# Kernel tuning notes

Hardware: AMD Instinct MI355X
Metric: run time of the kernel (lower is better)

Reference implementation:

```python
import jax, jax.numpy as jnp
import numpy as np

N = 1024          # n noisy tokens (seq = 2*N)
DIM = 768
HEADS = 12
HD = DIM // HEADS
BLOCK = 16        # diffusion block size
COND = 128
DFF = 4 * DIM
NEG = -1e30


def rotate_half(x):
    x1, x2 = jnp.split(x, 2, axis=-1)
    return jnp.concatenate((-x2, x1), axis=-1)


def layernorm(x):
    mu = jnp.mean(x, axis=-1, keepdims=True)
    var = jnp.var(x, axis=-1, keepdims=True)
    return (x - mu) * jax.lax.rsqrt(var + 1e-5)


def block_diff_mask(seq, n, block_size):
    idx = jnp.arange(seq)
    q_idx, kv_idx = idx[:, None], idx[None, :]
    fq = q_idx >= n
    fk = kv_idx >= n
    bq = jnp.where(fq, (q_idx - n) // block_size, q_idx // block_size)
    bk = jnp.where(fk, (kv_idx - n) // block_size, kv_idx // block_size)
    block_diagonal = (bq == bk) & (fq == fk)
    offset_block_causal = (bq > bk) & fk & (~fq)
    block_causal = (bq >= bk) & fk & fq
    return block_diagonal | offset_block_causal | block_causal  # [seq, seq] bool


def setup_inputs() -> dict:
    key = jax.random.key(0)
    ks = jax.random.split(key, 12)
    x = jax.random.normal(ks[0], (2, 2 * N, DIM), dtype=jnp.float32)
    c = jax.random.normal(ks[1], (2, COND), dtype=jnp.float32)
    # rotary tables over positions 0..N-1 (each half of the sequence reuses them)
    inv_freq = 1.0 / (10000.0 ** (jnp.arange(0, HD, 2, dtype=jnp.float32) / HD))
    freqs = jnp.arange(N, dtype=jnp.float32)[:, None] * inv_freq[None, :]  # [N, HD/2]
    emb = jnp.concatenate((freqs, freqs), axis=-1)  # [N, HD]
    cos, sin = jnp.cos(emb), jnp.sin(emb)
    s = 0.02
    W_qkv = jax.random.normal(ks[2], (DIM, 3 * DIM), dtype=jnp.float32) * s
    W_out = jax.random.normal(ks[3], (DIM, DIM), dtype=jnp.float32) * s
    ln1_w = jnp.ones((DIM,), dtype=jnp.float32)
    ln2_w = jnp.ones((DIM,), dtype=jnp.float32)
    mlp_w1 = jax.random.normal(ks[4], (DIM, DFF), dtype=jnp.float32) * s
    mlp_b1 = jnp.zeros((DFF,), dtype=jnp.float32)
    mlp_w2 = jax.random.normal(ks[5], (DFF, DIM), dtype=jnp.float32) * s
    mlp_b2 = jnp.zeros((DIM,), dtype=jnp.float32)
    ada_w = jax.random.normal(ks[6], (COND, 6 * DIM), dtype=jnp.float32) * s
    ada_b = jax.random.normal(ks[7], (6 * DIM,), dtype=jnp.float32) * s
    return {"x": x, "cos": cos, "sin": sin, "c": c, "W_qkv": W_qkv, "W_out": W_out,
            "ln1_w": ln1_w, "ln2_w": ln2_w, "mlp_w1": mlp_w1, "mlp_b1": mlp_b1,
            "mlp_w2": mlp_w2, "mlp_b2": mlp_b2, "ada_w": ada_w, "ada_b": ada_b}


def reference(x, cos, sin, c, W_qkv, W_out, ln1_w, ln2_w,
              mlp_w1, mlp_b1, mlp_w2, mlp_b2, ada_w, ada_b):
    b, seq, dim = x.shape
    n = seq // 2
    # adaLN modulation: [b, 1, dim] each (inference: dropout = identity)
    ada = (c @ ada_w + ada_b)[:, None, :]
    shift_msa, scale_msa, gate_msa, shift_mlp, scale_mlp, gate_mlp = jnp.split(ada, 6, axis=2)
    x_skip = x
    h = layernorm(x) * ln1_w
    h = h * (1.0 + scale_msa) + shift_msa  # modulate_fused

    def qkv_rope(seg):
        qkv = (seg @ W_qkv).reshape(b, n, 3, HEADS, HD)
        cs = cos[None, :, None, None, :]
        sn = sin[None, :, None, None, :]
        return qkv * cs + rotate_half(qkv) * sn

    # noisy half and clean (x0) half each get positions 0..n-1
    qkv = jnp.concatenate((qkv_rope(h[:, :n]), qkv_rope(h[:, n:])), axis=1)  # [b,2n,3,H,HD]
    q, k, v = qkv[:, :, 0], qkv[:, :, 1], qkv[:, :, 2]  # [b, 2n, H, HD]
    mask = block_diff_mask(seq, n, BLOCK)  # [2n, 2n]
    scores = jnp.einsum('bqhd,bkhd->bhqk', q, k) / jnp.sqrt(jnp.float32(HD))
    scores = jnp.where(mask[None, None], scores, NEG)
    attn = jax.nn.softmax(scores, axis=-1)
    o = jnp.einsum('bhqk,bkhd->bqhd', attn, v).reshape(b, seq, dim)
    # bias_dropout_add_scale (inference): gate * out + residual
    x1 = gate_msa * (o @ W_out) + x_skip
    h2 = layernorm(x1) * ln2_w
    h2 = h2 * (1.0 + scale_mlp) + shift_mlp
    mlp = jax.nn.gelu(h2 @ mlp_w1 + mlp_b1, approximate=True) @ mlp_w2 + mlp_b2
    return gate_mlp * mlp + x1
```

## Files before the change

kernel.cpp:

```cpp
#include <hip/hip_runtime.h>
#include <hip/hip_bf16.h>
#include <stdint.h>

#define DIM 768
#define SEQ 2048
#define TOKENS 4096
#define HEADS 12
#define DFF 3072
#define COND 128
#define ADA6 4608

typedef __attribute__((ext_vector_type(8))) short bf16x8;
typedef __attribute__((ext_vector_type(4))) float f32x4;

#define MFMA16x32(a, b, c) __builtin_amdgcn_mfma_f32_16x16x32_bf16(a, b, c, 0, 0, 0)
#define GLDS16(g, l)                                                                  \
    __builtin_amdgcn_global_load_lds((const __attribute__((address_space(1))) void*)(g), \
                                     (__attribute__((address_space(3))) void*)(l), 16, 0, 0)

__device__ __forceinline__ ushort f2bf(float f) {
    union { float f; uint32_t u; } v;
    v.f = f;
    uint32_t r = v.u + 0x7FFF + ((v.u >> 16) & 1);
    return (ushort)(r >> 16);
}

__device__ __forceinline__ uint32_t packbf2(float a, float b) {
    union { __hip_bfloat162 h; uint32_t u; } cv;
    cv.h = __float22bfloat162_rn(make_float2(a, b));
    return cv.u;
}

__global__ void ada_kernel(const float* __restrict__ c, const float* __restrict__ ada_w,
                           const float* __restrict__ ada_b, float* __restrict__ ada) {
    int j = blockIdx.x * 256 + threadIdx.x;
    int bb = blockIdx.y;
    if (j < ADA6) {
        float acc = ada_b[j];
        for (int k = 0; k < COND; ++k)
            acc = fmaf(c[bb * COND + k], ada_w[(long)k * ADA6 + j], acc);
        ada[bb * ADA6 + j] = acc;
    }
}

__global__ __launch_bounds__(256) void convT(const float* __restrict__ W,
                                             ushort* __restrict__ Wt, int K, int N) {
    __shared__ float t[64][65];
    int tid = threadIdx.x;
    int n0 = blockIdx.x * 64, k0 = blockIdx.y * 64;
#pragma unroll
    for (int it = 0; it < 4; ++it) {
        int idx = it * 256 + tid;
        int kr = idx >> 4, nc = (idx & 15) * 4;
        float4 v = *(const float4*)&W[(long)(k0 + kr) * N + n0 + nc];
        t[kr][nc] = v.x; t[kr][nc + 1] = v.y; t[kr][nc + 2] = v.z; t[kr][nc + 3] = v.w;
    }
    __syncthreads();
#pragma unroll
    for (int it = 0; it < 4; ++it) {
        int idx = it * 256 + tid;
        int nr = idx >> 4, kc = (idx & 15) * 4;
        ushort4 v;
        v.x = f2bf(t[kc][nr]); v.y = f2bf(t[kc + 1][nr]);
        v.z = f2bf(t[kc + 2][nr]); v.w = f2bf(t[kc + 3][nr]);
        *(ushort4*)&Wt[(long)(n0 + nr) * K + k0 + kc] = v;
    }
}

__global__ __launch_bounds__(256) void ln_mod_kernel(const float* __restrict__ x,
                                                     const float* __restrict__ w,
                                                     const float* __restrict__ ada,
                                                     int shiftOff, int scaleOff,
                                                     ushort* __restrict__ out) {
    int token = blockIdx.x;
    int bb = token >> 11;
    int tid = threadIdx.x;
    const float* xi = x + (long)token * DIM;
    float v[3];
    float sum = 0.f, sumsq = 0.f;
#pragma unroll
    for (int t = 0; t < 3; ++t) {
        float val = xi[tid + 256 * t];
        v[t] = val;
        sum += val;
        sumsq = fmaf(val, val, sumsq);
    }
    for (int msk = 1; msk < 64; msk <<= 1) {
        sum += __shfl_xor(sum, msk, 64);
        sumsq += __shfl_xor(sumsq, msk, 64);
    }
    __shared__ float red0[4], red1[4];
    int wave = tid >> 6;
    if ((tid & 63) == 0) { red0[wave] = sum; red1[wave] = sumsq; }
    __syncthreads();
    sum = red0[0] + red0[1] + red0[2] + red0[3];
    sumsq = red1[0] + red1[1] + red1[2] + red1[3];
    float mu = sum * (1.f / DIM);
    float var = sumsq * (1.f / DIM) - mu * mu;
    float rs = rsqrtf(var + 1e-5f);
    const float* sh = ada + bb * ADA6 + shiftOff;
    const float* sc = ada + bb * ADA6 + scaleOff;
    ushort* oi = out + (long)token * DIM;
#pragma unroll
    for (int t = 0; t < 3; ++t) {
        int j = tid + 256 * t;
        oi[j] = f2bf((v[t] - mu) * rs * w[j] * (1.f + sc[j]) + sh[j]);
    }
}

template <int EPI, int BM>
__global__ __launch_bounds__(256) void gemm_bf16(const ushort* __restrict__ A,
                                                 const ushort* __restrict__ B,
                                                 void* __restrict__ Cp, int M, int N, int K,
                                                 const float* __restrict__ bias,
                                                 const float* __restrict__ gate,
                                                 const float* __restrict__ skip,
                                                 const float* __restrict__ cosT,
                                                 const float* __restrict__ sinT) {
    constexpr int MR = BM / 32;
    __shared__ ushort As[BM * 64];
    __shared__ ushort Bs[128 * 64];
    const int tid = threadIdx.x;
    const int wave = tid >> 6, lane = tid & 63;
    const int lo = lane & 15, hi = lane >> 4;
    const int wr = wave >> 1, wc = wave & 1;
    const int row0 = blockIdx.y * BM, col0 = blockIdx.x * 128;
    const int srow = tid >> 3;
    const int scol = (tid & 7) * 8;
    f32x4 acc[MR][4] = {};
    const long astep = (long)32 * K;
    const ushort* Ag = A + (long)(row0 + srow) * K + scol;
    const ushort* Bg = B + (long)(col0 + srow) * K + scol;
    for (int k0 = 0; k0 < K; k0 += 64) {
        __syncthreads();
#pragma unroll
        for (int t = 0; t < MR; ++t)
            GLDS16(Ag + t * astep + k0, (char*)As + (t * 256 + tid) * 16);
#pragma unroll
        for (int t = 0; t < 4; ++t)
            GLDS16(Bg + t * astep + k0, (char*)Bs + (t * 256 + tid) * 16);
        __syncthreads();
#pragma unroll
        for (int kk = 0; kk < 2; ++kk) {
            bf16x8 af[MR], bfr[4];
#pragma unroll
            for (int m = 0; m < MR; ++m)
                af[m] = *(const bf16x8*)&As[(wr * (BM / 2) + m * 16 + lo) * 64 + kk * 32 + hi * 8];
#pragma unroll
            for (int n = 0; n < 4; ++n)
                bfr[n] = *(const bf16x8*)&Bs[(wc * 64 + n * 16 + lo) * 64 + kk * 32 + hi * 8];
#pragma unroll
            for (int m = 0; m < MR; ++m)
#pragma unroll
                for (int n = 0; n < 4; ++n)
                    acc[m][n] = MFMA16x32(af[m], bfr[n], acc[m][n]);
        }
    }
    if (EPI == 0) {
        ushort* C = (ushort*)Cp;
#pragma unroll
        for (int m = 0; m < MR; ++m)
#pragma unroll
            for (int reg = 0; reg < 4; ++reg) {
                int r = row0 + wr * (BM / 2) + m * 16 + hi * 4 + reg;
                int pos = r & 1023;
                const float* cb = cosT + pos * 64;
                const float* sb = sinT + pos * 64;
                long rb = (long)r * N + col0 + wc * 64;
#pragma unroll
                for (int pr = 0; pr < 2; ++pr) {
                    int i = pr * 16 + lo;
                    float v0 = acc[m][pr][reg], v1 = acc[m][pr + 2][reg];
                    float c0 = cb[i], s0 = sb[i], c1 = cb[i + 32], s1 = sb[i + 32];
                    C[rb + i] = f2bf(v0 * c0 - v1 * s0);
                    C[rb + i + 32] = f2bf(v1 * c1 + v0 * s1);
                }
            }
    } else if (EPI == 1) {
        float* C = (float*)Cp;
#pragma unroll
        for (int m = 0; m < MR; ++m)
#pragma unroll
            for (int reg = 0; reg < 4; ++reg) {
                int r = row0 + wr * (BM / 2) + m * 16 + hi * 4 + reg;
                int bbi = r >> 11;
#pragma unroll
                for (int n = 0; n < 4; ++n) {
                    int c = col0 + wc * 64 + n * 16 + lo;
                    C[(long)r * N + c] =
                        gate[bbi * ADA6 + c] * acc[m][n][reg] + skip[(long)r * DIM + c];
                }
            }
    } else if (EPI == 2) {
        ushort* C = (ushort*)Cp;
#pragma unroll
        for (int m = 0; m < MR; ++m)
#pragma unroll
            for (int reg = 0; reg < 4; ++reg) {
                int r = row0 + wr * (BM / 2) + m * 16 + hi * 4 + reg;
#pragma unroll
                for (int n = 0; n < 4; ++n) {
                    int c = col0 + wc * 64 + n * 16 + lo;
                    float v = acc[m][n][reg] + bias[c];
                    float g = v / (1.f + __expf(-1.5957691216f * (v + 0.044715f * v * v * v)));
                    C[(long)r * N + c] = f2bf(g);
                }
            }
    } else {
        float* C = (float*)Cp;
#pragma unroll
        for (int m = 0; m < MR; ++m)
#pragma unroll
            for (int reg = 0; reg < 4; ++reg) {
                int r = row0 + wr * (BM / 2) + m * 16 + hi * 4 + reg;
                int bbi = r >> 11;
#pragma unroll
                for (int n = 0; n < 4; ++n) {
                    int c = col0 + wc * 64 + n * 16 + lo;
                    C[(long)r * N + c] = gate[bbi * ADA6 + c] * (acc[m][n][reg] + bias[c]) +
                                         skip[(long)r * DIM + c];
                }
            }
    }
}

__global__ __launch_bounds__(256) void vtrans(const ushort* __restrict__ qkv,
                                              ushort* __restrict__ vt) {
    __shared__ ushort t[64][65];
    int tid = threadIdx.x;
    int tb = blockIdx.x;
    int head = blockIdx.y;
    int bb = blockIdx.z;
#pragma unroll
    for (int it = 0; it < 4; ++it) {
        int idx = it * 256 + tid;
        int tok = idx >> 4, d4 = (idx & 15) * 4;
        const ushort* p = qkv + ((long)bb * SEQ + tb * 64 + tok) * 2304 + 1536 + head * 64 + d4;
        ushort4 v = *(const ushort4*)p;
        t[tok][d4] = v.x; t[tok][d4 + 1] = v.y; t[tok][d4 + 2] = v.z; t[tok][d4 + 3] = v.w;
    }
    __syncthreads();
#pragma unroll
    for (int it = 0; it < 4; ++it) {
        int idx = it * 256 + tid;
        int d = idx >> 4, t4 = (idx & 15) * 4;
        ushort4 v;
        v.x = t[t4][d]; v.y = t[t4 + 1][d]; v.z = t[t4 + 2][d]; v.w = t[t4 + 3][d];
        *(ushort4*)&vt[((long)(bb * HEADS + head) * 64 + d) * SEQ + tb * 64 + t4] = v;
    }
}

__global__ __launch_bounds__(256) void attn_mfma(const ushort* __restrict__ qkv,
                                                 const ushort* __restrict__ vt,
                                                 ushort* __restrict__ o) {
    __shared__ ushort Ks[2][4096];
    __shared__ ushort Vs[2][4096];
    __shared__ char ps[4][2048];
    const int tid = threadIdx.x;
    const int wave = tid >> 6, lane = tid & 63;
    const int lo = lane & 15, hi = lane >> 4;
    const int bx = blockIdx.x;
    const int tile = (bx & 1) ? (31 - (bx >> 1)) : (15 - (bx >> 1));
    const int head = blockIdx.y;
    const int bb = blockIdx.z;
    char* psb = ps[wave];
    const int swz = (lo & 7) << 4;
    const bool fh = tile < 16;
    const int ncausal = fh ? ((tile * 64 + 111) >> 6) : (tile - 15);
    const int nchunks = ncausal + (fh ? 1 : 0);
    const int q0 = tile * 64 + wave * 16;
    const int vcaus = fh ? q0 : (q0 - 1024 + 16);
    const long row0 = (long)bb * SEQ + q0;

    const ushort* Qp = qkv + (row0 + lo) * 2304 + head * 64 + hi * 8;
    bf16x8 qf0 = *(const bf16x8*)Qp;
    bf16x8 qf1 = *(const bf16x8*)(Qp + 32);
    f32x4 oacc[4] = {};
    float m_run = -3.0e38f, l_run = 0.f;

    const int srow = tid >> 3;
    const int sc8 = tid & 7;
    const ushort* Kg = qkv + ((long)bb * SEQ) * 2304 + DIM + head * 64;
    const ushort* Vg = vt + ((long)(bb * HEADS + head) * 64) * SEQ;

    auto STAGE = [&](int buf, int kbase) {
#pragma unroll
        for (int it = 0; it < 2; ++it) {
            int r = it * 32 + srow;
            int c8 = sc8 ^ (r & 7);
            GLDS16(Kg + (long)(kbase + r) * 2304 + c8 * 8,
                   (char*)Ks[buf] + it * 4096 + tid * 16);
        }
#pragma unroll
        for (int it = 0; it < 2; ++it) {
            int r = it * 32 + srow;
            int c8 = sc8 ^ (r & 7);
            GLDS16(Vg + (long)r * SEQ + kbase + c8 * 8,
                   (char*)Vs[buf] + it * 4096 + tid * 16);
        }
    };
#define KB(cc) (((cc) < ncausal) ? (1024 + (cc) * 64) : (tile * 64))

    STAGE(0, KB(0));
    for (int c = 0; c < nchunks; ++c) {
        const int cur = c & 1;
        if (c + 1 < nchunks) {
            STAGE(1 - cur, KB(c + 1));
            asm volatile("s_waitcnt vmcnt(4)" ::: "memory");
        } else {
            asm volatile("s_waitcnt vmcnt(0)" ::: "memory");
        }
        __builtin_amdgcn_s_barrier();
        __builtin_amdgcn_sched_barrier(0);
        const bool isdiag = (c >= ncausal);
        const int v = isdiag ? 16 : (vcaus - c * 64);
        if (v > 0) {
            f32x4 s4[4];
#pragma unroll
            for (int n = 0; n < 4; ++n) {
                f32x4 z = {};
#pragma unroll
                for (int kk = 0; kk < 2; ++kk) {
                    const bf16x8 kf = *(const bf16x8*)((const char*)Ks[cur] +
                        ((n * 16 + lo) << 7) + ((((kk << 2) + hi) ^ (lo & 7)) << 4));
                    z = MFMA16x32(kf, kk ? qf1 : qf0, z);
                }
                s4[n] = z;
            }
            const int vv = isdiag ? 64 : min(v, 64);
            float p[4][4];
            float mx = -3.0e38f;
#pragma unroll
            for (int n = 0; n < 4; ++n)
#pragma unroll
                for (int g = 0; g < 4; ++g) {
                    bool ok = isdiag ? (n == wave) : (n * 16 + hi * 4 + g < vv);
                    float val = ok ? s4[n][g] * 0.125f : -3.0e38f;
                    p[n][g] = val;
                    mx = fmaxf(mx, val);
                }
            mx = fmaxf(mx, __shfl_xor(mx, 16, 64));
            mx = fmaxf(mx, __shfl_xor(mx, 32, 64));
            float m_new = fmaxf(m_run, mx);
            float scale = __expf(m_run - m_new);
            float psum = 0.f;
#pragma unroll
            for (int n = 0; n < 4; ++n)
#pragma unroll
                for (int g = 0; g < 4; ++g) {
                    float e = __expf(p[n][g] - m_new);
                    p[n][g] = e;
                    psum += e;
                }
            psum += __shfl_xor(psum, 16, 64);
            psum += __shfl_xor(psum, 32, 64);
            l_run = l_run * scale + psum;
            m_run = m_new;
#pragma unroll
            for (int dt = 0; dt < 4; ++dt) oacc[dt] *= scale;
#pragma unroll
            for (int n = 0; n < 4; ++n)
#pragma unroll
                for (int pr = 0; pr < 2; ++pr) {
                    uint32_t u = packbf2(p[n][pr * 2], p[n][pr * 2 + 1]);
                    *(uint32_t*)(psb + lo * 128 + ((n * 32 + hi * 8 + pr * 4) ^ swz)) = u;
                }
            bf16x8 pa0 = *(const bf16x8*)(psb + lo * 128 + ((hi * 16) ^ swz));
            bf16x8 pa1 = *(const bf16x8*)(psb + lo * 128 + ((64 + hi * 16) ^ swz));
#pragma unroll
            for (int dt = 0; dt < 4; ++dt) {
#pragma unroll
                for (int kk = 0; kk < 2; ++kk) {
                    const bf16x8 vf = *(const bf16x8*)((const char*)Vs[cur] +
                        ((dt * 16 + lo) << 7) + ((((kk << 2) + hi) ^ (lo & 7)) << 4));
                    oacc[dt] = MFMA16x32(vf, kk ? pa1 : pa0, oacc[dt]);
                }
            }
        }
        __builtin_amdgcn_s_barrier();
        __builtin_amdgcn_sched_barrier(0);
    }
#undef KB

    float inv = 1.f / l_run;
#pragma unroll
    for (int dt = 0; dt < 4; ++dt) {
        ushort4 st;
        st.x = f2bf(oacc[dt][0] * inv);
        st.y = f2bf(oacc[dt][1] * inv);
        st.z = f2bf(oacc[dt][2] * inv);
        st.w = f2bf(oacc[dt][3] * inv);
        *(ushort4*)&o[(row0 + lo) * DIM + head * 64 + dt * 16 + hi * 4] = st;
    }
}

extern "C" void kernel_launch(void* const* d_in, const int* in_sizes, int n_in,
                              void* d_out, int out_size, void* d_ws, size_t ws_size,
                              hipStream_t stream) {
    const float* x      = (const float*)d_in[0];
    const float* cosT   = (const float*)d_in[1];
    const float* sinT   = (const float*)d_in[2];
    const float* c      = (const float*)d_in[3];
    const float* W_qkv  = (const float*)d_in[4];
    const float* W_out  = (const float*)d_in[5];
    const float* ln1_w  = (const float*)d_in[6];
    const float* ln2_w  = (const float*)d_in[7];
    const float* mlp_w1 = (const float*)d_in[8];
    const float* mlp_b1 = (const float*)d_in[9];
    const float* mlp_w2 = (const float*)d_in[10];
    const float* mlp_b2 = (const float*)d_in[11];
    const float* ada_w  = (const float*)d_in[12];
    const float* ada_b  = (const float*)d_in[13];
    float* out = (float*)d_out;

    char* ws = (char*)d_ws;
    float*  ada   = (float*)(ws + 0);
    ushort* h     = (ushort*)(ws + 65536L);
    ushort* qkv   = (ushort*)(ws + 6356992L);
    ushort* vt    = (ushort*)(ws + 25231360L);
    ushort* o     = (ushort*)(ws + 31522816L);
    float*  x1    = (float*)(ws + 37814272L);
    ushort* a1    = (ushort*)(ws + 50397184L);
    ushort* wqkvT = (ushort*)(ws + 75563008L);
    ushort* woutT = (ushort*)(ws + 79101952L);
    ushort* w1T   = (ushort*)(ws + 80281600L);
    ushort* w2T   = (ushort*)(ws + 85000192L);

    ada_kernel<<<dim3(18, 2), 256, 0, stream>>>(c, ada_w, ada_b, ada);
    convT<<<dim3(36, 12), 256, 0, stream>>>(W_qkv, wqkvT, 768, 2304);
    convT<<<dim3(12, 12), 256, 0, stream>>>(W_out, woutT, 768, 768);
    convT<<<dim3(48, 12), 256, 0, stream>>>(mlp_w1, w1T, 768, 3072);
    convT<<<dim3(12, 48), 256, 0, stream>>>(mlp_w2, w2T, 3072, 768);

    ln_mod_kernel<<<TOKENS, 256, 0, stream>>>(x, ln1_w, ada, 0, 768, h);
    gemm_bf16<0, 128><<<dim3(18, 32), 256, 0, stream>>>(h, wqkvT, qkv, TOKENS, 2304, 768,
                                                        nullptr, nullptr, nullptr, cosT, sinT);
    vtrans<<<dim3(32, 12, 2), 256, 0, stream>>>(qkv, vt);
    attn_mfma<<<dim3(32, 12, 2), 256, 0, stream>>>(qkv, vt, o);
    gemm_bf16<1, 64><<<dim3(6, 64), 256, 0, stream>>>(o, woutT, x1, TOKENS, 768, 768,
                                                      nullptr, ada + 1536, x, nullptr, nullptr);
    ln_mod_kernel<<<TOKENS, 256, 0, stream>>>(x1, ln2_w, ada, 2304, 3072, h);
    gemm_bf16<2, 128><<<dim3(24, 32), 256, 0, stream>>>(h, w1T, a1, TOKENS, DFF, 768,
                                                        mlp_b1, nullptr, nullptr, nullptr, nullptr);
    gemm_bf16<3, 64><<<dim3(6, 64), 256, 0, stream>>>(a1, w2T, out, TOKENS, 768, DFF,
                                                      mlp_b2, ada + 3840, x1, nullptr, nullptr);
}
```

Before: 327.5 us.

## Double-buffer GEMM LDS tiles and swizzle workgroup order for L2 reuse

The bf16 GEMM now uses two LDS buffers per operand, issuing the global-to-LDS loads for the next K tile before computing on the current one and waiting with explicit vmcnt counts instead of full syncthreads. This lets memory latency overlap with MFMA work. The workgroup index is also remapped across groups of eight to change which tiles run together, aiming for better cache reuse. LDS usage doubles, which can lower occupancy, and the hand-tuned vmcnt values must match the number of loads per stage and the hardware's in-order completion.

Result: faster. 319.5 us (-2.5%).

```diff
diff --git a/kernel.cpp b/kernel.cpp
--- a/kernel.cpp
+++ b/kernel.cpp
@@ -118,43 +118,65 @@
                                                  const float* __restrict__ cosT,
                                                  const float* __restrict__ sinT) {
     constexpr int MR = BM / 32;
-    __shared__ ushort As[BM * 64];
-    __shared__ ushort Bs[128 * 64];
+    __shared__ ushort As[2][BM * 64];
+    __shared__ ushort Bs[2][128 * 64];
     const int tid = threadIdx.x;
     const int wave = tid >> 6, lane = tid & 63;
     const int lo = lane & 15, hi = lane >> 4;
     const int wr = wave >> 1, wc = wave & 1;
-    const int row0 = blockIdx.y * BM, col0 = blockIdx.x * 128;
+    const int gx = gridDim.x;
+    const int nwg = gx * gridDim.y;
+    const int flat = blockIdx.y * gx + blockIdx.x;
+    const int swzid = (flat & 7) * (nwg >> 3) + (flat >> 3);
+    const int row0 = (swzid / gx) * BM, col0 = (swzid % gx) * 128;
     const int srow = tid >> 3;
     const int scol = (tid & 7) * 8;
     f32x4 acc[MR][4] = {};
     const long astep = (long)32 * K;
     const ushort* Ag = A + (long)(row0 + srow) * K + scol;
     const ushort* Bg = B + (long)(col0 + srow) * K + scol;
-    for (int k0 = 0; k0 < K; k0 += 64) {
-        __syncthreads();
+
+    auto STAGE = [&](int buf, int kt) {
+        const int k0 = kt * 64;
 #pragma unroll
         for (int t = 0; t < MR; ++t)
-            GLDS16(Ag + t * astep + k0, (char*)As + (t * 256 + tid) * 16);
+            GLDS16(Ag + t * astep + k0, (char*)As[buf] + (t * 256 + tid) * 16);
 #pragma unroll
         for (int t = 0; t < 4; ++t)
-            GLDS16(Bg + t * astep + k0, (char*)Bs + (t * 256 + tid) * 16);
-        __syncthreads();
+            GLDS16(Bg + t * astep + k0, (char*)Bs[buf] + (t * 256 + tid) * 16);
+    };
+
+    const int nkt = K >> 6;
+    STAGE(0, 0);
+    for (int kt = 0; kt < nkt; ++kt) {
+        const int cur = kt & 1;
+        if (kt + 1 < nkt) {
+            STAGE(1 - cur, kt + 1);
+            if constexpr (BM == 128)
+                asm volatile("s_waitcnt vmcnt(8)" ::: "memory");
+            else
+                asm volatile("s_waitcnt vmcnt(6)" ::: "memory");
+        } else {
+            asm volatile("s_waitcnt vmcnt(0)" ::: "memory");
+        }
+        __builtin_amdgcn_s_barrier();
+        __builtin_amdgcn_sched_barrier(0);
 #pragma unroll
         for (int kk = 0; kk < 2; ++kk) {
             bf16x8 af[MR], bfr[4];
 #pragma unroll
             for (int m = 0; m < MR; ++m)
-                af[m] = *(const bf16x8*)&As[(wr * (BM / 2) + m * 16 + lo) * 64 + kk * 32 + hi * 8];
+                af[m] = *(const bf16x8*)&As[cur][(wr * (BM / 2) + m * 16 + lo) * 64 + kk * 32 + hi * 8];
 #pragma unroll
             for (int n = 0; n < 4; ++n)
-                bfr[n] = *(const bf16x8*)&Bs[(wc * 64 + n * 16 + lo) * 64 + kk * 32 + hi * 8];
+                bfr[n] = *(const bf16x8*)&Bs[cur][(wc * 64 + n * 16 + lo) * 64 + kk * 32 + hi * 8];
 #pragma unroll
             for (int m = 0; m < MR; ++m)
 #pragma unroll
                 for (int n = 0; n < 4; ++n)
                     acc[m][n] = MFMA16x32(af[m], bfr[n], acc[m][n]);
         }
+        __builtin_amdgcn_s_barrier();
     }
     if (EPI == 0) {
         ushort* C = (ushort*)Cp;
```
